# Kernel tuning notes

Hardware: AMD Instinct MI355X
Metric: run time of the kernel (lower is better)

Reference implementation:

```python
import jax, jax.numpy as jnp
import numpy as np
from jax import lax

B, T, F, L, H, KT, HOR = 32, 12, 2, 1024, 64, 1, 12


def setup_inputs() -> dict:
    key = jax.random.key(0)
    ks = jax.random.split(key, 18)
    stdv = 1.0 / np.sqrt(H)
    u = lambda k, s: jax.random.uniform(k, s, jnp.float32, -stdv, stdv)
    return {
        "x": jax.random.normal(ks[0], (B, T, F * L), jnp.float32),
        "input_attn_w": 0.01 * (jax.random.uniform(ks[1], (L, L), jnp.float32) - 0.5),
        "hidden_attn_w": 0.01 * (jax.random.uniform(ks[2], (L, L), jnp.float32) - 0.5),
        "reset_hidden_weight": u(ks[3], (L, H, H)),
        "reset_hidden_bias": u(ks[4], (H, L)),
        "reset_input_weight": u(ks[5], (L, F, H)),
        "reset_input_bias": u(ks[6], (H, L)),
        "update_hidden_weight": u(ks[7], (L, H, H)),
        "update_hidden_bias": u(ks[8], (H, L)),
        "update_input_weight": u(ks[9], (L, F, H)),
        "update_input_bias": u(ks[10], (H, L)),
        "new_hidden_weight": u(ks[11], (L, H, H)),
        "new_hidden_bias": u(ks[12], (H, L)),
        "new_input_weight": u(ks[13], (L, F, H)),
        "new_input_bias": u(ks[14], (H, L)),
        "fc_weight": u(ks[15], (L, H, KT)),
        "fc_bias": u(ks[16], (KT, L)),
    }


def reference(x, input_attn_w, hidden_attn_w,
              reset_hidden_weight, reset_hidden_bias,
              reset_input_weight, reset_input_bias,
              update_hidden_weight, update_hidden_bias,
              update_input_weight, update_input_bias,
              new_hidden_weight, new_hidden_bias,
              new_input_weight, new_input_bias,
              fc_weight, fc_bias):
    Bx = x.shape[0]

    def attn(v, W):  # nn.Linear(L, L, bias=False) on last axis: v @ W.T
        return jnp.einsum('bcl,ml->bcm', v, W)

    def prop(hidden, in_i):
        # hidden: [B, H, L]; in_i: [B, F, L]; per-link batched gate GEMMs
        gh = lambda W, b: jnp.einsum('bhl,lhk->bkl', hidden, W) + b
        gi = lambda W, b: jnp.einsum('bfl,lfk->bkl', in_i, W) + b
        r = jax.nn.sigmoid(gh(reset_hidden_weight, reset_hidden_bias)
                           + gi(reset_input_weight, reset_input_bias))
        z = jax.nn.sigmoid(gh(update_hidden_weight, update_hidden_bias)
                           + gi(update_input_weight, update_input_bias))
        n = jnp.tanh(r * gh(new_hidden_weight, new_hidden_bias)
                     + gi(new_input_weight, new_input_bias))
        return (1.0 - z) * n + z * hidden

    def enc_step(hidden, x_t):
        in_i = attn(x_t.reshape(Bx, F, L), input_attn_w)
        hidden = attn(hidden, hidden_attn_w)
        return prop(hidden, in_i), None

    h0 = jnp.zeros((Bx, H, L), x.dtype)
    hidden, _ = lax.scan(enc_step, h0, jnp.swapaxes(x, 0, 1))

    def dec_step(hidden, _):
        out_i = jnp.einsum('bhl,lhk->bkl', hidden, fc_weight) + fc_bias  # [B, KT, L]
        # source_feature[0] is the target feature, source_feature[1] is not
        in_i = jnp.concatenate([out_i, jnp.zeros_like(out_i)], axis=1)  # [B, F, L]
        in_i = attn(in_i, input_attn_w)
        hidden = attn(hidden, hidden_attn_w)
        return prop(hidden, in_i), out_i.reshape(Bx, KT * L)

    _, outs = lax.scan(dec_step, hidden, None, length=HOR)
    return jnp.swapaxes(outs, 0, 1)  # [B, HOR, KT*L]
```

## Files before the change

### kernel.cpp

```cpp
#include <hip/hip_runtime.h>

#define T_ 12
#define L_ 1024
#define H_ 64
#define HOR_ 12
#define BH_ 2048

typedef unsigned short u16;
typedef __attribute__((ext_vector_type(8))) __bf16 bf16x8;
typedef __attribute__((ext_vector_type(8))) u16 u16x8;
typedef __attribute__((ext_vector_type(4))) float f32x4;

__device__ __forceinline__ u16 f2b(float f) {
  union { float f; unsigned u; } v; v.f = f;
  unsigned r = v.u + 0x7FFFu + ((v.u >> 16) & 1u);
  return (u16)(r >> 16);
}
__device__ __forceinline__ float b2f(u16 b) {
  union { unsigned u; float f; } v; v.u = ((unsigned)b) << 16;
  return v.f;
}
__device__ __forceinline__ void gld16(const void* g, void* l) {
  __builtin_amdgcn_global_load_lds((const __attribute__((address_space(1))) void*)g,
                                   (__attribute__((address_space(3))) void*)l, 16, 0, 0);
}


__global__ __launch_bounds__(256) void k_prep(
    const float* __restrict__ Wh, const float* __restrict__ Wi, const float* __restrict__ x,
    u16* __restrict__ WhT, u16* __restrict__ Wib, u16* __restrict__ xb,
    const float* __restrict__ Wr, const float* __restrict__ Wz, const float* __restrict__ Wn,
    u16* __restrict__ WTr, u16* __restrict__ WTz, u16* __restrict__ WTn,
    const float* __restrict__ brh, const float* __restrict__ bri,
    const float* __restrict__ bzh, const float* __restrict__ bzi,
    const float* __restrict__ bnh, const float* __restrict__ bni,
    float* __restrict__ BRZ, float* __restrict__ BZZ,
    float* __restrict__ BNH, float* __restrict__ BNI) {
  __shared__ u16 lds[64][66];
  const int bid = blockIdx.x, tid = threadIdx.x;
  if (bid < 1792) {
    const float* in; u16* out; int i;
    if (bid < 1024) { in = Wi; out = Wib; i = bid * 256 + tid; }
    else            { in = x;  out = xb;  i = (bid - 1024) * 256 + tid; }
    float4 v = ((const float4*)in)[i];
    ushort4 o;
    o.x = f2b(v.x); o.y = f2b(v.y); o.z = f2b(v.z); o.w = f2b(v.w);
    ((ushort4*)out)[i] = o;
  } else if (bid < 2048) {
    const int q = bid - 1792;
    const int mt = q >> 4, kt = q & 15;
    u16* dst = WhT + (size_t)(mt * 16 + kt) * 4096;
#pragma unroll
    for (int j = 0; j < 2; ++j) {
      int ci = j * 256 + tid;
      int ln = ci & 63, kt2 = (ci >> 6) & 1, uu = (ci >> 7) & 1, gh = (ci >> 8) & 1;
      int rw = gh * 32 + uu * 16 + (ln & 15);
      int cw0 = kt2 * 32 + (ln >> 4) * 8;
      const float* src = Wh + (size_t)(mt * 64 + rw) * 1024 + kt * 64 + cw0;
      float4 v0 = *(const float4*)src, v1 = *(const float4*)(src + 4);
      u16x8 o;
      o[0] = f2b(v0.x); o[1] = f2b(v0.y); o[2] = f2b(v0.z); o[3] = f2b(v0.w);
      o[4] = f2b(v1.x); o[5] = f2b(v1.y); o[6] = f2b(v1.z); o[7] = f2b(v1.w);
      *(u16x8*)(dst + ci * 8) = o;
    }
  } else if (bid < 5120) {
    const int q = bid - 2048;
    const int sel = q >> 10, l = q & 1023;
    const float* w = (sel == 0 ? Wr : sel == 1 ? Wz : Wn) + (size_t)l * 4096;
    u16* t = (sel == 0 ? WTr : sel == 1 ? WTz : WTn) + (size_t)l * 4096;
#pragma unroll
    for (int j = 0; j < 16; ++j) {
      int idx = j * 256 + tid;
      lds[idx & 63][idx >> 6] = f2b(w[idx]);
    }
    __syncthreads();
#pragma unroll
    for (int j = 0; j < 2; ++j) {
      int w8 = j * 256 + tid;
      int k = w8 >> 3, h0 = (w8 & 7) * 8;
      u16x8 v;
#pragma unroll
      for (int e = 0; e < 8; ++e) v[e] = lds[k][h0 + e];
      *(u16x8*)(t + k * 64 + h0) = v;
    }
  } else {
    const int idx = (bid - 5120) * 256 + tid;
    const int l = idx >> 6, k = idx & 63;
    const int i = k * 1024 + l, o = l * 64 + k;
    BRZ[o] = brh[i] + bri[i];
    BZZ[o] = bzh[i] + bzi[i];
    BNH[o] = bnh[i];
    BNI[o] = bni[i];
  }
}

__global__ __launch_bounds__(256) void k_gemm_t(const u16* __restrict__ WhT,
                                                const u16* __restrict__ HbT,
                                                u16* __restrict__ C) {
  __shared__ __align__(16) u16 lA[4096];
  __shared__ __align__(16) u16 lB[4096];
  const int tid = threadIdx.x;
  const int lane = tid & 63, wv = tid >> 6;
  const int mt = blockIdx.y, nt = blockIdx.x;
  const int gA = wv >> 1, gB = wv & 1;
  const int r16 = lane & 15, q4 = lane >> 4;
  const u16* srcA = WhT + (size_t)mt * 16 * 4096;
  const u16* srcB = HbT + (size_t)nt * 16 * 4096;
  f32x4 acc[2][2] = {};
  for (int s = 0; s < 16; ++s) {
    __syncthreads();
#pragma unroll
    for (int j = 0; j < 2; ++j) {
      int ci = j * 256 + tid;
      gld16(srcA + (size_t)s * 4096 + ci * 8, lA + ci * 8);
      gld16(srcB + (size_t)s * 4096 + ci * 8, lB + ci * 8);
    }
    __syncthreads();
#pragma unroll
    for (int kt = 0; kt < 2; ++kt) {
      bf16x8 af[2], bfv[2];
#pragma unroll
      for (int u = 0; u < 2; ++u) {
        af[u]  = *(const bf16x8*)&lA[((gA * 2 + u) * 2 + kt) * 512 + lane * 8];
        bfv[u] = *(const bf16x8*)&lB[((gB * 2 + u) * 2 + kt) * 512 + lane * 8];
      }
#pragma unroll
      for (int i = 0; i < 2; ++i)
#pragma unroll
        for (int j = 0; j < 2; ++j)
          acc[i][j] = __builtin_amdgcn_mfma_f32_16x16x32_bf16(af[i], bfv[j], acc[i][j], 0, 0, 0);
    }
  }
#pragma unroll
  for (int i = 0; i < 2; ++i)
#pragma unroll
    for (int j = 0; j < 2; ++j)
#pragma unroll
      for (int e = 0; e < 4; ++e) {
        size_t row = mt * 64 + gA * 32 + i * 16 + q4 * 4 + e;
        size_t col = nt * 64 + gB * 32 + j * 16 + r16;
        C[row * BH_ + col] = f2b(acc[i][j][e]);
      }
}

__global__ __launch_bounds__(256) void k_gemm_nt(const u16* __restrict__ A,
                                                 const u16* __restrict__ Bm,
                                                 float* __restrict__ C, int N, int K) {
  __shared__ __align__(16) u16 lA[64 * 64];
  __shared__ __align__(16) u16 lB[128 * 64];
  const int tid = threadIdx.x;
  const int lane = tid & 63, wv = tid >> 6;
  const int m0 = blockIdx.y * 64, n0 = blockIdx.x * 128;
  const int g2 = wv >> 1, gb = wv & 1;
  const int wm = g2 * 32, wn = gb * 64;
  const int r16 = lane & 15, q4 = lane >> 4;
  f32x4 acc[2][4] = {};
  for (int k0 = 0; k0 < K; k0 += 64) {
    __syncthreads();
#pragma unroll
    for (int j = 0; j < 2; ++j) {
      int ci = j * 256 + tid;
      int ln = ci & 63, kt = (ci >> 6) & 1, u = (ci >> 7) & 1, g = ci >> 8;
      int row = g * 32 + u * 16 + (ln & 15), c = kt * 4 + ((ln >> 4) & 3);
      gld16(A + (size_t)(m0 + row) * K + k0 + c * 8, lA + ci * 8);
    }
#pragma unroll
    for (int j = 0; j < 4; ++j) {
      int ci = j * 256 + tid;
      int ln = ci & 63, kt = (ci >> 6) & 1, u = (ci >> 7) & 3, g = ci >> 9;
      int row = g * 64 + u * 16 + (ln & 15), c = kt * 4 + ((ln >> 4) & 3);
      gld16(Bm + (size_t)(n0 + row) * K + k0 + c * 8, lB + ci * 8);
    }
    __syncthreads();
#pragma unroll
    for (int kt = 0; kt < 2; ++kt) {
      bf16x8 af[2], bfv[4];
#pragma unroll
      for (int u = 0; u < 2; ++u)
        af[u] = *(const bf16x8*)&lA[((g2 * 2 + u) * 2 + kt) * 512 + lane * 8];
#pragma unroll
      for (int u = 0; u < 4; ++u)
        bfv[u] = *(const bf16x8*)&lB[((gb * 4 + u) * 2 + kt) * 512 + lane * 8];
#pragma unroll
      for (int i = 0; i < 2; ++i)
#pragma unroll
        for (int j = 0; j < 4; ++j)
          acc[i][j] = __builtin_amdgcn_mfma_f32_16x16x32_bf16(af[i], bfv[j], acc[i][j], 0, 0, 0);
    }
  }
#pragma unroll
  for (int i = 0; i < 2; ++i)
#pragma unroll
    for (int j = 0; j < 4; ++j)
#pragma unroll
      for (int e = 0; e < 4; ++e) {
        size_t row = m0 + wm + i * 16 + q4 * 4 + e;
        size_t col = n0 + wn + j * 16 + r16;
        C[row * N + col] = acc[i][j][e];
      }
}

template <int ENC, int Z, int FC>
__global__ __launch_bounds__(512, 4) void k_gates(
    const u16* __restrict__ Aalt, const u16* __restrict__ WTr, const u16* __restrict__ WTz,
    const u16* __restrict__ WTn, const float* __restrict__ BRZ, const float* __restrict__ BZZ,
    const float* __restrict__ BNH, const float* __restrict__ BNI,
    const float* __restrict__ Wir, const float* __restrict__ Wiz, const float* __restrict__ Win,
    const float* __restrict__ inp, const u16* __restrict__ OUTFC_r, const u16* __restrict__ Wib,
    const float* __restrict__ fcw, const float* __restrict__ fcb,
    float* __restrict__ outp, u16* __restrict__ OUTFC_w, int t, int s_out,
    u16* __restrict__ HbT) {
  __shared__ __align__(8) u16 lout[BH_ * 2];
  __shared__ __align__(16) u16 lWi[2048];
  __shared__ float din[2][2][32];
  const int tid = threadIdx.x;
  const int lane = tid & 63, wv = tid >> 6;
  const int li = wv >> 2, mh = (wv >> 1) & 1, nh = wv & 1;
  const int bid = blockIdx.x;
  const int wg = (bid & 7) * 64 + (bid >> 3);
  const int l = wg * 2 + li;
  const int r16 = lane & 15, q4 = lane >> 4;

  if (ENC) {
    if (tid < 128) {
      int b = tid & 31, f = (tid >> 5) & 1, li2 = tid >> 6;
      din[li2][f][b] = inp[(((size_t)b * T_ + t) * 2 + f) * L_ + wg * 2 + li2];
    }
    __syncthreads();
  } else {
    if (tid < 256) ((uint4*)lWi)[tid] = ((const uint4*)(Wib + (size_t)(wg * 2) * 1024))[tid];
    __syncthreads();
    const int pair = tid >> 3, sub = tid & 7;
    const int pb = pair >> 1, pl = pair & 1;
    const u16* orow = OUTFC_r + pb * 1024 + sub * 128;
    const u16* wrow = lWi + pl * 1024 + sub * 128;
    float s = 0.f;
#pragma unroll
    for (int j = 0; j < 16; ++j) {
      u16x8 o = *(const u16x8*)(orow + j * 8);
      u16x8 w = *(const u16x8*)(wrow + j * 8);
#pragma unroll
      for (int e = 0; e < 8; ++e) s += b2f(o[e]) * b2f(w[e]);
    }
    s += __shfl_xor(s, 1); s += __shfl_xor(s, 2); s += __shfl_xor(s, 4);
    if (sub == 0) { din[pl][0][pb] = s; din[pl][1][pb] = 0.f; }
    __syncthreads();
  }

  const u16* al = Aalt + (size_t)l * BH_;
  bf16x8 a[2];
  f32x4 aR[2] = {}, aZ[2] = {}, aN[2] = {};
  if (Z == 0) {
#pragma unroll
    for (int kt = 0; kt < 2; ++kt)
      a[kt] = *(const bf16x8*)&al[(mh * 16 + r16) * 64 + kt * 32 + q4 * 8];
    const size_t wbase = (size_t)l * 4096 + (size_t)(nh * 32 + r16) * 64 + q4 * 8;
#define DO_GATE(W, acc)                                                              \
    {                                                                                \
      bf16x8 w00 = *(const bf16x8*)&W[wbase];                                        \
      bf16x8 w01 = *(const bf16x8*)&W[wbase + 32];                                   \
      bf16x8 w10 = *(const bf16x8*)&W[wbase + 1024];                                 \
      bf16x8 w11 = *(const bf16x8*)&W[wbase + 1024 + 32];                            \
      acc[0] = __builtin_amdgcn_mfma_f32_16x16x32_bf16(a[0], w00, acc[0], 0, 0, 0);  \
      acc[0] = __builtin_amdgcn_mfma_f32_16x16x32_bf16(a[1], w01, acc[0], 0, 0, 0);  \
      acc[1] = __builtin_amdgcn_mfma_f32_16x16x32_bf16(a[0], w10, acc[1], 0, 0, 0);  \
      acc[1] = __builtin_amdgcn_mfma_f32_16x16x32_bf16(a[1], w11, acc[1], 0, 0, 0);  \
    }
    DO_GATE(WTr, aR)
    DO_GATE(WTz, aZ)
    DO_GATE(WTn, aN)
#undef DO_GATE
  }

  float i0v[4], i1v[4];
#pragma unroll
  for (int e = 0; e < 4; ++e) {
    const int bb = mh * 16 + q4 * 4 + e;
    i0v[e] = din[li][0][bb];
    i1v[e] = ENC ? din[li][1][bb] : 0.f;
  }
#pragma unroll
  for (int ntl = 0; ntl < 2; ++ntl) {
    const int kk = nh * 32 + ntl * 16 + r16;
    const float vbr  = BRZ[l * 64 + kk];
    const float vbz  = BZZ[l * 64 + kk];
    const float vbnh = BNH[l * 64 + kk];
    const float vbni = BNI[l * 64 + kk];
    const float wr0 = Wir[l * 128 + kk], wr1 = Wir[l * 128 + 64 + kk];
    const float wz0 = Wiz[l * 128 + kk], wz1 = Wiz[l * 128 + 64 + kk];
    const float wn0 = Win[l * 128 + kk], wn1 = Win[l * 128 + 64 + kk];
#pragma unroll
    for (int e = 0; e < 4; ++e) {
      const int bb = mh * 16 + q4 * 4 + e;
      const float i0 = i0v[e], i1 = i1v[e];
      const float gr = aR[ntl][e] + vbr + i0 * wr0 + i1 * wr1;
      const float gz = aZ[ntl][e] + vbz + i0 * wz0 + i1 * wz1;
      const float gnh = aN[ntl][e] + vbnh;
      const float gni = i0 * wn0 + i1 * wn1 + vbni;
      const float rr = 1.f / (1.f + __expf(-gr));
      const float zz = 1.f / (1.f + __expf(-gz));
      const float xx = rr * gnh + gni;
      const float ex = __expf(2.f * xx);
      const float nn = (ex - 1.f) / (ex + 1.f);
      const float av = Z ? 0.f : b2f(al[bb * 64 + kk]);
      lout[(bb * 64 + kk) * 2 + li] = f2b((1.f - zz) * nn + zz * av);
    }
  }
  __syncthreads();

  {
    const int c0 = wg * 2;
    const int ktile = c0 >> 6;
    const int cw = c0 & 63;
    const int kt2 = cw >> 5, q = (cw >> 3) & 3, e = cw & 7;
    for (int i = tid; i < BH_; i += 512) {
      int rw = i & 63, nt = i >> 6;
      int ci = (((rw >> 5) * 2 + ((rw >> 4) & 1)) * 2 + kt2) * 64 + (rw & 15) + q * 16;
      *(unsigned*)(HbT + (size_t)(nt * 16 + ktile) * 4096 + ci * 8 + e) =
          *(const unsigned*)&lout[i * 2];
    }
  }

  if (FC) {
    if (tid < 64) {
      const int b = tid & 31, li2 = tid >> 5;
      const int lf = wg * 2 + li2;
      float acc = 0.f;
      const float* wp = fcw + (size_t)lf * 64;
#pragma unroll 8
      for (int hh = 0; hh < 64; ++hh) {
        int h = (hh + b) & 63;
        acc += b2f(lout[(b * 64 + h) * 2 + li2]) * wp[h];
      }
      acc += fcb[lf];
      outp[((size_t)b * HOR_ + s_out) * L_ + lf] = acc;
      OUTFC_w[(size_t)b * 1024 + lf] = f2b(acc);
    }
  }
}

#define WS_HT    (size_t)0
#define WS_AALT  ((size_t)4 << 20)
#define WS_WHT   ((size_t)8 << 20)
#define WS_WIB   ((size_t)10 << 20)
#define WS_XB    ((size_t)12 << 20)
#define WS_WTR   ((size_t)14 << 20)
#define WS_WTZ   ((size_t)22 << 20)
#define WS_WTN   ((size_t)30 << 20)
#define WS_ENCIN ((size_t)38 << 20)
#define WS_OFC0  ((size_t)41 << 20)
#define WS_OFC1  (((size_t)41 << 20) + (64 << 10))
#define WS_BRZ   ((size_t)42 << 20)
#define WS_BZZ   (((size_t)42 << 20) + (256 << 10))
#define WS_BNH   (((size_t)42 << 20) + (512 << 10))
#define WS_BNI   (((size_t)42 << 20) + (768 << 10))

extern "C" void kernel_launch(void* const* d_in, const int* in_sizes, int n_in,
                              void* d_out, int out_size, void* d_ws, size_t ws_size,
                              hipStream_t stream) {
  const float* x   = (const float*)d_in[0];
  const float* Wi  = (const float*)d_in[1];
  const float* Wh  = (const float*)d_in[2];
  const float* Wrh = (const float*)d_in[3];
  const float* brh = (const float*)d_in[4];
  const float* Wri = (const float*)d_in[5];
  const float* bri = (const float*)d_in[6];
  const float* Wzh = (const float*)d_in[7];
  const float* bzh = (const float*)d_in[8];
  const float* Wzi = (const float*)d_in[9];
  const float* bzi = (const float*)d_in[10];
  const float* Wnh = (const float*)d_in[11];
  const float* bnh = (const float*)d_in[12];
  const float* Wni = (const float*)d_in[13];
  const float* bni = (const float*)d_in[14];
  const float* fcw = (const float*)d_in[15];
  const float* fcb = (const float*)d_in[16];
  float* out = (float*)d_out;

  char* ws = (char*)d_ws;
  u16*   HbT   = (u16*)(ws + WS_HT);
  u16*   Aalt  = (u16*)(ws + WS_AALT);
  u16*   WhT   = (u16*)(ws + WS_WHT);
  u16*   Wib   = (u16*)(ws + WS_WIB);
  u16*   xb    = (u16*)(ws + WS_XB);
  u16*   WTr   = (u16*)(ws + WS_WTR);
  u16*   WTz   = (u16*)(ws + WS_WTZ);
  u16*   WTn   = (u16*)(ws + WS_WTN);
  float* ENCIN = (float*)(ws + WS_ENCIN);
  u16*   OFC0  = (u16*)(ws + WS_OFC0);
  u16*   OFC1  = (u16*)(ws + WS_OFC1);
  float* BRZ   = (float*)(ws + WS_BRZ);
  float* BZZ   = (float*)(ws + WS_BZZ);
  float* BNH   = (float*)(ws + WS_BNH);
  float* BNI   = (float*)(ws + WS_BNI);

  k_prep<<<5376, 256, 0, stream>>>(Wh, Wi, x, WhT, Wib, xb, Wrh, Wzh, Wnh, WTr, WTz, WTn,
                                   brh, bri, bzh, bzi, bnh, bni, BRZ, BZZ, BNH, BNI);
  k_gemm_nt<<<dim3(8, 12), 256, 0, stream>>>(xb, Wib, ENCIN, 1024, 1024);

  k_gates<1, 1, 0><<<512, 512, 0, stream>>>(Aalt, WTr, WTz, WTn, BRZ, BZZ, BNH, BNI,
                                            Wri, Wzi, Wni, ENCIN, OFC0, Wib, fcw, fcb,
                                            out, OFC0, 0, 0, HbT);
  for (int t = 1; t < T_; ++t) {
    k_gemm_t<<<dim3(32, 16), 256, 0, stream>>>(WhT, HbT, Aalt);
    if (t < T_ - 1)
      k_gates<1, 0, 0><<<512, 512, 0, stream>>>(Aalt, WTr, WTz, WTn, BRZ, BZZ, BNH, BNI,
                                                Wri, Wzi, Wni, ENCIN, OFC0, Wib, fcw, fcb,
                                                out, OFC0, t, 0, HbT);
    else
      k_gates<1, 0, 1><<<512, 512, 0, stream>>>(Aalt, WTr, WTz, WTn, BRZ, BZZ, BNH, BNI,
                                                Wri, Wzi, Wni, ENCIN, OFC0, Wib, fcw, fcb,
                                                out, OFC0, t, 0, HbT);
  }
  for (int s = 0; s <= 10; ++s) {
    const u16* ofr = (s & 1) ? OFC1 : OFC0;
    u16*       ofw = (s & 1) ? OFC0 : OFC1;
    k_gemm_t<<<dim3(32, 16), 256, 0, stream>>>(WhT, HbT, Aalt);
    k_gates<0, 0, 1><<<512, 512, 0, stream>>>(Aalt, WTr, WTz, WTn, BRZ, BZZ, BNH, BNI,
                                              Wri, Wzi, Wni, ENCIN, ofr, Wib, fcw, fcb,
                                              out, ofw, 0, s + 1, HbT);
  }
}
```

Baseline: 725.2 us.

## Enlarge hidden-attention GEMM tiles to 128x128 and skip final hidden writeback

The recurrent hidden-attention GEMM moves from 64x64 output tiles (512 blocks) to 128x128 tiles (128 blocks). Each wave now computes a 64x64 sub-tile with a 4x4 MFMA accumulator set, which raises operand reuse from LDS and cuts global reloads of the weight and hidden panels. The pre-packed weight and hidden layouts are changed to a flat 16-row grouping to match the new tiling. A template flag also drops the hidden-state writeback in the last decoder step, whose result is never read. The trade-off is fewer blocks than CUs on a large GPU and higher register and LDS use per block.

```diff
diff --git a/kernel.cpp b/kernel.cpp
--- a/kernel.cpp
+++ b/kernel.cpp
@@ -53,8 +53,8 @@
 #pragma unroll
     for (int j = 0; j < 2; ++j) {
       int ci = j * 256 + tid;
-      int ln = ci & 63, kt2 = (ci >> 6) & 1, uu = (ci >> 7) & 1, gh = (ci >> 8) & 1;
-      int rw = gh * 32 + uu * 16 + (ln & 15);
+      int ln = ci & 63, kt2 = (ci >> 6) & 1, g = (ci >> 7) & 3;
+      int rw = g * 16 + (ln & 15);
       int cw0 = kt2 * 32 + (ln >> 4) * 8;
       const float* src = Wh + (size_t)(mt * 64 + rw) * 1024 + kt * 64 + cw0;
       float4 v0 = *(const float4*)src, v1 = *(const float4*)(src + 4);
@@ -94,51 +94,52 @@
   }
 }
 
-__global__ __launch_bounds__(256) void k_gemm_t(const u16* __restrict__ WhT,
-                                                const u16* __restrict__ HbT,
-                                                u16* __restrict__ C) {
-  __shared__ __align__(16) u16 lA[4096];
-  __shared__ __align__(16) u16 lB[4096];
+__global__ __launch_bounds__(256, 2) void k_gemm_t(const u16* __restrict__ WhT,
+                                                   const u16* __restrict__ HbT,
+                                                   u16* __restrict__ C) {
+  __shared__ __align__(16) u16 lA[2][4096];
+  __shared__ __align__(16) u16 lB[2][4096];
   const int tid = threadIdx.x;
   const int lane = tid & 63, wv = tid >> 6;
-  const int mt = blockIdx.y, nt = blockIdx.x;
-  const int gA = wv >> 1, gB = wv & 1;
+  const int NT = blockIdx.x, MT = blockIdx.y;
+  const int wm = wv & 1, wn = wv >> 1;
   const int r16 = lane & 15, q4 = lane >> 4;
-  const u16* srcA = WhT + (size_t)mt * 16 * 4096;
-  const u16* srcB = HbT + (size_t)nt * 16 * 4096;
-  f32x4 acc[2][2] = {};
+  f32x4 acc[4][4] = {};
   for (int s = 0; s < 16; ++s) {
     __syncthreads();
 #pragma unroll
-    for (int j = 0; j < 2; ++j) {
+    for (int j = 0; j < 8; ++j) {
       int ci = j * 256 + tid;
-      gld16(srcA + (size_t)s * 4096 + ci * 8, lA + ci * 8);
-      gld16(srcB + (size_t)s * 4096 + ci * 8, lB + ci * 8);
+      int sub = ci >> 9, off = ci & 511;
+      if (sub < 2)
+        gld16(WhT + (size_t)((MT * 2 + sub) * 16 + s) * 4096 + off * 8, lA[sub] + off * 8);
+      else
+        gld16(HbT + (size_t)((NT * 2 + (sub - 2)) * 16 + s) * 4096 + off * 8, lB[sub - 2] + off * 8);
     }
     __syncthreads();
 #pragma unroll
     for (int kt = 0; kt < 2; ++kt) {
-      bf16x8 af[2], bfv[2];
-#pragma unroll
-      for (int u = 0; u < 2; ++u) {
-        af[u]  = *(const bf16x8*)&lA[((gA * 2 + u) * 2 + kt) * 512 + lane * 8];
-        bfv[u] = *(const bf16x8*)&lB[((gB * 2 + u) * 2 + kt) * 512 + lane * 8];
+      bf16x8 af[4], bfv[4];
+#pragma unroll
+      for (int u = 0; u < 4; ++u) {
+        af[u]  = *(const bf16x8*)&lA[wm][(u * 2 + kt) * 512 + lane * 8];
+        bfv[u] = *(const bf16x8*)&lB[wn][(u * 2 + kt) * 512 + lane * 8];
       }
 #pragma unroll
-      for (int i = 0; i < 2; ++i)
-#pragma unroll
-        for (int j = 0; j < 2; ++j)
+      for (int i = 0; i < 4; ++i)
+#pragma unroll
+        for (int j = 0; j < 4; ++j)
           acc[i][j] = __builtin_amdgcn_mfma_f32_16x16x32_bf16(af[i], bfv[j], acc[i][j], 0, 0, 0);
     }
   }
 #pragma unroll
-  for (int i = 0; i < 2; ++i)
-#pragma unroll
-    for (int j = 0; j < 2; ++j)
+  for (int i = 0; i < 4; ++i)
+#pragma unroll
+    for (int j = 0; j < 4; ++j)
 #pragma unroll
       for (int e = 0; e < 4; ++e) {
-        size_t row = mt * 64 + gA * 32 + i * 16 + q4 * 4 + e;
-        size_t col = nt * 64 + gB * 32 + j * 16 + r16;
+        size_t row = MT * 128 + wm * 64 + i * 16 + q4 * 4 + e;
+        size_t col = NT * 128 + wn * 64 + j * 16 + r16;
         C[row * BH_ + col] = f2b(acc[i][j][e]);
       }
 }
@@ -200,7 +201,7 @@
       }
 }
 
-template <int ENC, int Z, int FC>
+template <int ENC, int Z, int FC, int WH>
 __global__ __launch_bounds__(512, 4) void k_gates(
     const u16* __restrict__ Aalt, const u16* __restrict__ WTr, const u16* __restrict__ WTz,
     const u16* __restrict__ WTn, const float* __restrict__ BRZ, const float* __restrict__ BZZ,
@@ -308,14 +309,14 @@
   }
   __syncthreads();
 
-  {
+  if (WH) {
     const int c0 = wg * 2;
     const int ktile = c0 >> 6;
     const int cw = c0 & 63;
     const int kt2 = cw >> 5, q = (cw >> 3) & 3, e = cw & 7;
     for (int i = tid; i < BH_; i += 512) {
       int rw = i & 63, nt = i >> 6;
-      int ci = (((rw >> 5) * 2 + ((rw >> 4) & 1)) * 2 + kt2) * 64 + (rw & 15) + q * 16;
+      int ci = ((rw >> 4) * 2 + kt2) * 64 + (rw & 15) + q * 16;
       *(unsigned*)(HbT + (size_t)(nt * 16 + ktile) * 4096 + ci * 8 + e) =
           *(const unsigned*)&lout[i * 2];
     }
@@ -398,26 +399,31 @@
                                    brh, bri, bzh, bzi, bnh, bni, BRZ, BZZ, BNH, BNI);
   k_gemm_nt<<<dim3(8, 12), 256, 0, stream>>>(xb, Wib, ENCIN, 1024, 1024);
 
-  k_gates<1, 1, 0><<<512, 512, 0, stream>>>(Aalt, WTr, WTz, WTn, BRZ, BZZ, BNH, BNI,
-                                            Wri, Wzi, Wni, ENCIN, OFC0, Wib, fcw, fcb,
-                                            out, OFC0, 0, 0, HbT);
+  k_gates<1, 1, 0, 1><<<512, 512, 0, stream>>>(Aalt, WTr, WTz, WTn, BRZ, BZZ, BNH, BNI,
+                                               Wri, Wzi, Wni, ENCIN, OFC0, Wib, fcw, fcb,
+                                               out, OFC0, 0, 0, HbT);
   for (int t = 1; t < T_; ++t) {
-    k_gemm_t<<<dim3(32, 16), 256, 0, stream>>>(WhT, HbT, Aalt);
+    k_gemm_t<<<dim3(16, 8), 256, 0, stream>>>(WhT, HbT, Aalt);
     if (t < T_ - 1)
-      k_gates<1, 0, 0><<<512, 512, 0, stream>>>(Aalt, WTr, WTz, WTn, BRZ, BZZ, BNH, BNI,
-                                                Wri, Wzi, Wni, ENCIN, OFC0, Wib, fcw, fcb,
-                                                out, OFC0, t, 0, HbT);
+      k_gates<1, 0, 0, 1><<<512, 512, 0, stream>>>(Aalt, WTr, WTz, WTn, BRZ, BZZ, BNH, BNI,
+                                                   Wri, Wzi, Wni, ENCIN, OFC0, Wib, fcw, fcb,
+                                                   out, OFC0, t, 0, HbT);
     else
-      k_gates<1, 0, 1><<<512, 512, 0, stream>>>(Aalt, WTr, WTz, WTn, BRZ, BZZ, BNH, BNI,
-                                                Wri, Wzi, Wni, ENCIN, OFC0, Wib, fcw, fcb,
-                                                out, OFC0, t, 0, HbT);
+      k_gates<1, 0, 1, 1><<<512, 512, 0, stream>>>(Aalt, WTr, WTz, WTn, BRZ, BZZ, BNH, BNI,
+                                                   Wri, Wzi, Wni, ENCIN, OFC0, Wib, fcw, fcb,
+                                                   out, OFC0, t, 0, HbT);
   }
   for (int s = 0; s <= 10; ++s) {
     const u16* ofr = (s & 1) ? OFC1 : OFC0;
     u16*       ofw = (s & 1) ? OFC0 : OFC1;
-    k_gemm_t<<<dim3(32, 16), 256, 0, stream>>>(WhT, HbT, Aalt);
-    k_gates<0, 0, 1><<<512, 512, 0, stream>>>(Aalt, WTr, WTz, WTn, BRZ, BZZ, BNH, BNI,
-                                              Wri, Wzi, Wni, ENCIN, ofr, Wib, fcw, fcb,
-                                              out, ofw, 0, s + 1, HbT);
-  }
-}
+    k_gemm_t<<<dim3(16, 8), 256, 0, stream>>>(WhT, HbT, Aalt);
+    if (s < 10)
+      k_gates<0, 0, 1, 1><<<512, 512, 0, stream>>>(Aalt, WTr, WTz, WTn, BRZ, BZZ, BNH, BNI,
+                                                   Wri, Wzi, Wni, ENCIN, ofr, Wib, fcw, fcb,
+                                                   out, ofw, 0, s + 1, HbT);
+    else
+      k_gates<0, 0, 1, 0><<<512, 512, 0, stream>>>(Aalt, WTr, WTz, WTn, BRZ, BZZ, BNH, BNI,
+                                                   Wri, Wzi, Wni, ENCIN, ofr, Wib, fcw, fcb,
+                                                   out, ofw, 0, s + 1, HbT);
+  }
+}
```

Result: slower. 885.7 us (+22.1%).
